# Optimization experiments

Measured on AMD Instinct MI355X. Metric: run time of the kernel, lower is better.

The kernel has to match this reference:

```python
import jax, jax.numpy as jnp
import numpy as np

B = 16384      # batch
F = 26         # onehot fields
E = 32         # embedding_dim
L = 50         # multihot bag length
V = 1000000    # num_embeddings
CT = 13        # continuous features
D0, D1, D2, D3 = 909, 512, 256, 1
LEAKY = 0.01


def _leaky(x):
    return jnp.where(x >= 0, x, LEAKY * x)


def setup_inputs() -> dict:
    key = jax.random.key(0)
    ks = jax.random.split(key, 16)
    inp = {
        "onehot_i": jax.random.randint(ks[0], (B, F), 0, V),
        "onehot_x": jax.random.uniform(ks[1], (B, F), dtype=jnp.float32),
        "multihot_i1": jax.random.randint(ks[2], (B, L), 0, V),
        "multihot_x1": jax.random.uniform(ks[3], (B, L), dtype=jnp.float32),
        "multihot_i2": jax.random.randint(ks[4], (B, L), 0, V),
        "multihot_x2": jax.random.uniform(ks[5], (B, L), dtype=jnp.float32),
        "ctns": jax.random.normal(ks[6], (B, CT), dtype=jnp.float32),
        # learned parameters
        "wide_table": jax.random.normal(ks[7], (V, 1), dtype=jnp.float32) * 0.02,
        "deep_table": jax.random.normal(ks[8], (V, E), dtype=jnp.float32) * 0.02,
        "w2": jax.random.normal(ks[9], (D1, D0), dtype=jnp.float32) * (1.0 / np.sqrt(D0)),
        "b2": jnp.zeros((D1,), dtype=jnp.float32),
        "w3": jax.random.normal(ks[10], (D2, D1), dtype=jnp.float32) * (1.0 / np.sqrt(D1)),
        "b3": jnp.zeros((D2,), dtype=jnp.float32),
        "w4": jax.random.normal(ks[11], (D3, D2), dtype=jnp.float32) * (1.0 / np.sqrt(D2)),
        "b4": jnp.zeros((D3,), dtype=jnp.float32),
    }
    return inp


def reference(onehot_i, onehot_x, multihot_i1, multihot_x1, multihot_i2,
              multihot_x2, ctns, wide_table, deep_table, w2, b2, w3, b3, w4, b4):
    # ---- wide part ----
    # Original broadcasts the [B,F,1] wide embedding against x repeated E times,
    # then sums over all columns. That equals E * sum_f(w[idx]*x).
    wide_sum = (wide_table[onehot_i, 0] * onehot_x).sum(axis=1)          # [B]
    wide_sum = wide_sum + (wide_table[multihot_i1, 0] * multihot_x1).sum(axis=1)
    wide_sum = wide_sum + (wide_table[multihot_i2, 0] * multihot_x2).sum(axis=1)
    wide_out = E * wide_sum                                              # [B]

    # ---- deep part: gather, scale by field weight, pool multihot bags ----
    d_one = (deep_table[onehot_i] * onehot_x[:, :, None]).reshape(B, F * E)   # [B, F*E]
    d_m1 = (deep_table[multihot_i1] * multihot_x1[:, :, None]).sum(axis=1)    # [B, E]
    d_m2 = (deep_table[multihot_i2] * multihot_x2[:, :, None]).sum(axis=1)    # [B, E]
    x = jnp.concatenate([d_one, d_m1, d_m2, ctns], axis=1)                    # [B, D0]

    # dropout p=0.0 (deterministic reference)
    x = _leaky(x @ w2.T + b2)
    x = _leaky(x @ w3.T + b3)
    x = (x @ w4.T + b4).squeeze(-1)                                           # [B]
    return jax.nn.sigmoid(x + wide_out)
```

## Files before the change

kernel.cpp:

```cpp
#include <hip/hip_runtime.h>
#include <hip/hip_bf16.h>
#include <math.h>

#define B_   16384
#define F_   26
#define E_   32
#define L_   50
#define CT_  13
#define D0_  909
#define D0P  928
#define D1_  512
#define D2_  256

typedef __bf16 bf16x8 __attribute__((ext_vector_type(8)));
typedef float f32x4 __attribute__((ext_vector_type(4)));

__device__ inline float bf2f(unsigned short u) {
    union { unsigned int i; float f; } v; v.i = ((unsigned int)u) << 16; return v.f;
}
__device__ inline unsigned short f2b(float f) {
    union { __hip_bfloat16 h; unsigned short u; } v;
    v.h = __float2bfloat16(f);
    return v.u;
}

__device__ inline void gld_lds16(const void* g, void* l) {
    __builtin_amdgcn_global_load_lds(
        (const __attribute__((address_space(1))) unsigned int*)g,
        (__attribute__((address_space(3))) unsigned int*)l, 16, 0, 0);
}

#define W2N (D1_ * D0P)
#define W3N (D2_ * D1_)
__global__ __launch_bounds__(256) void cvt_weights(
    const float* __restrict__ w2, const float* __restrict__ w3,
    __hip_bfloat16* __restrict__ o2, __hip_bfloat16* __restrict__ o3)
{
    int i = blockIdx.x * 256 + threadIdx.x;
    if (i < W2N) {
        int r = i / D0P, c = i - r * D0P;
        float v = (c < D0_) ? w2[r * D0_ + c] : 0.f;
        o2[i] = __float2bfloat16(v);
    } else {
        int j = i - W2N;
        if (j < W3N) o3[j] = __float2bfloat16(w3[j]);
    }
}

__global__ __launch_bounds__(256, 4) void embed_kernel(
    const int* __restrict__ oi, const float* __restrict__ ox,
    const int* __restrict__ i1, const float* __restrict__ x1,
    const int* __restrict__ i2, const float* __restrict__ x2,
    const float* __restrict__ ct, const float* __restrict__ wtab,
    const float* __restrict__ dtab,
    __hip_bfloat16* __restrict__ x0, float* __restrict__ wide)
{
    const int s    = blockIdx.x * 4 + (threadIdx.x >> 6);
    const int lane = threadIdx.x & 63;
    const int g    = lane >> 3;
    const int l    = lane & 7;
    unsigned short* xrow = (unsigned short*)(x0 + (size_t)s * D0P);
    const f32x4* dt4 = (const f32x4*)dtab;

    int koh[4]; float soh[4];
#pragma unroll
    for (int t = 0; t < 4; t++) {
        int f = g + 8 * t; bool v = (f < F_);
        koh[t] = v ? oi[s * F_ + f] : 0;
        soh[t] = v ? ox[s * F_ + f] : 0.f;
    }
    int k1[7], k2[7]; float sc1[7], sc2[7];
#pragma unroll
    for (int t = 0; t < 7; t++) {
        int j = g + 8 * t; bool v = (j < L_);
        k1[t]  = v ? i1[s * L_ + j] : 0;
        sc1[t] = v ? x1[s * L_ + j] : 0.f;
        k2[t]  = v ? i2[s * L_ + j] : 0;
        sc2[t] = v ? x2[s * L_ + j] : 0.f;
    }

    f32x4 r1[7], r2[7], roh[4];
#pragma unroll
    for (int t = 0; t < 7; t++) r1[t] = dt4[(size_t)k1[t] * 8 + l];
#pragma unroll
    for (int t = 0; t < 7; t++) r2[t] = dt4[(size_t)k2[t] * 8 + l];
#pragma unroll
    for (int t = 0; t < 4; t++) roh[t] = dt4[(size_t)koh[t] * 8 + l];

#pragma unroll
    for (int t = 0; t < 4; t++) {
        int f = g + 8 * t;
        if (f < F_) {
            ushort4 o;
            o.x = f2b(roh[t].x * soh[t]); o.y = f2b(roh[t].y * soh[t]);
            o.z = f2b(roh[t].z * soh[t]); o.w = f2b(roh[t].w * soh[t]);
            *(ushort4*)(xrow + f * E_ + l * 4) = o;
        }
    }

    f32x4 a1 = {0.f,0.f,0.f,0.f}, a2 = {0.f,0.f,0.f,0.f};
#pragma unroll
    for (int t = 0; t < 7; t++) {
        a1.x = fmaf(r1[t].x, sc1[t], a1.x); a1.y = fmaf(r1[t].y, sc1[t], a1.y);
        a1.z = fmaf(r1[t].z, sc1[t], a1.z); a1.w = fmaf(r1[t].w, sc1[t], a1.w);
        a2.x = fmaf(r2[t].x, sc2[t], a2.x); a2.y = fmaf(r2[t].y, sc2[t], a2.y);
        a2.z = fmaf(r2[t].z, sc2[t], a2.z); a2.w = fmaf(r2[t].w, sc2[t], a2.w);
    }
#pragma unroll
    for (int m = 8; m < 64; m <<= 1) {
        a1.x += __shfl_xor(a1.x, m); a1.y += __shfl_xor(a1.y, m);
        a1.z += __shfl_xor(a1.z, m); a1.w += __shfl_xor(a1.w, m);
        a2.x += __shfl_xor(a2.x, m); a2.y += __shfl_xor(a2.y, m);
        a2.z += __shfl_xor(a2.z, m); a2.w += __shfl_xor(a2.w, m);
    }
    if (g == 0) {
        ushort4 o; o.x = f2b(a1.x); o.y = f2b(a1.y); o.z = f2b(a1.z); o.w = f2b(a1.w);
        *(ushort4*)(xrow + F_ * E_ + l * 4) = o;
    }
    if (g == 1) {
        ushort4 o; o.x = f2b(a2.x); o.y = f2b(a2.y); o.z = f2b(a2.z); o.w = f2b(a2.w);
        *(ushort4*)(xrow + F_ * E_ + E_ + l * 4) = o;
    }
    if (lane < E_) {
        float v = (lane < CT_) ? ct[s * CT_ + lane] : 0.f;
        xrow[F_ * E_ + 2 * E_ + lane] = f2b(v);
    }
    float acc = 0.f;
#pragma unroll
    for (int t = lane; t < F_ + 2 * L_; t += 64) {
        int idx; float xv;
        if (t < F_)            { idx = oi[s * F_ + t];            xv = ox[s * F_ + t]; }
        else if (t < F_ + L_)  { int j = t - F_;       idx = i1[s * L_ + j]; xv = x1[s * L_ + j]; }
        else                   { int j = t - F_ - L_;  idx = i2[s * L_ + j]; xv = x2[s * L_ + j]; }
        acc += wtab[idx] * xv;
    }
    for (int o = 32; o; o >>= 1) acc += __shfl_xor(acc, o);
    if (lane == 0) wide[s] = (float)E_ * acc;
}

template<int N, int K, bool ACT>
__global__ __launch_bounds__(256) void gemm_bias(
    const __hip_bfloat16* __restrict__ A,
    const __hip_bfloat16* __restrict__ W,
    const float* __restrict__ bias,
    __hip_bfloat16* __restrict__ C, int MBLKS)
{
    __shared__ __hip_bfloat16 As[128 * 32];
    __shared__ __hip_bfloat16 Bs[128 * 32];

    const int bm   = blockIdx.x % MBLKS;
    const int bn   = blockIdx.x / MBLKS;
    const int tid  = threadIdx.x;
    const int lane = tid & 63;
    const int w    = tid >> 6;
    const int wm   = w >> 1, wn = w & 1;

    f32x4 acc[4][4] = {};

    const int srow = lane >> 2;
    const int scol = (lane & 3) * 8;
    const __hip_bfloat16* Aw0 = A + ((size_t)bm * 128 + w * 32 + srow) * K + scol;
    const __hip_bfloat16* Aw1 = Aw0 + (size_t)16 * K;
    const __hip_bfloat16* Ww0 = W + ((size_t)bn * 128 + w * 32 + srow) * K + scol;
    const __hip_bfloat16* Ww1 = Ww0 + (size_t)16 * K;
    char* AsW = (char*)As + w * 2048;
    char* BsW = (char*)Bs + w * 2048;

    const int fr = lane & 15;
    const int kg = (lane >> 4) * 8;

    for (int k0 = 0; k0 < K; k0 += 32) {
        gld_lds16(Aw0 + k0, AsW);
        gld_lds16(Aw1 + k0, AsW + 1024);
        gld_lds16(Ww0 + k0, BsW);
        gld_lds16(Ww1 + k0, BsW + 1024);
        __syncthreads();

        bf16x8 af[4], bfv[4];
#pragma unroll
        for (int i = 0; i < 4; i++)
            af[i] = *(const bf16x8*)(As + (wm * 64 + i * 16 + fr) * 32 + kg);
#pragma unroll
        for (int i = 0; i < 4; i++)
            bfv[i] = *(const bf16x8*)(Bs + (wn * 64 + i * 16 + fr) * 32 + kg);
#pragma unroll
        for (int i = 0; i < 4; i++)
#pragma unroll
            for (int j = 0; j < 4; j++)
                acc[i][j] = __builtin_amdgcn_mfma_f32_16x16x32_bf16(af[i], bfv[j], acc[i][j], 0, 0, 0);
        __syncthreads();
    }

    float bv[4];
#pragma unroll
    for (int j = 0; j < 4; j++) bv[j] = bias[bn * 128 + wn * 64 + j * 16 + fr];
    const int crow0 = bm * 128 + wm * 64 + (lane >> 4) * 4;
    const int ccol0 = bn * 128 + wn * 64 + fr;
#pragma unroll
    for (int i = 0; i < 4; i++)
#pragma unroll
        for (int j = 0; j < 4; j++)
#pragma unroll
            for (int r = 0; r < 4; r++) {
                float v = acc[i][j][r] + bv[j];
                if (ACT) v = (v >= 0.f) ? v : 0.01f * v;
                C[(size_t)(crow0 + i * 16 + r) * N + ccol0 + j * 16] = __float2bfloat16(v);
            }
}

__global__ __launch_bounds__(256) void final_kernel(
    const __hip_bfloat16* __restrict__ h2, const float* __restrict__ w4,
    const float* __restrict__ b4, const float* __restrict__ wide,
    float* __restrict__ out)
{
    const int s    = blockIdx.x * 4 + (threadIdx.x >> 6);
    const int lane = threadIdx.x & 63;
    const unsigned short* hp = (const unsigned short*)(h2 + (size_t)s * D2_);
    ushort4 hv = *(const ushort4*)(hp + lane * 4);
    float4  wv = *(const float4*)(w4 + lane * 4);
    float acc = bf2f(hv.x) * wv.x + bf2f(hv.y) * wv.y + bf2f(hv.z) * wv.z + bf2f(hv.w) * wv.w;
    for (int o = 32; o; o >>= 1) acc += __shfl_xor(acc, o);
    if (lane == 0) {
        float x = acc + b4[0] + wide[s];
        out[s] = 1.f / (1.f + expf(-x));
    }
}

extern "C" void kernel_launch(void* const* d_in, const int* in_sizes, int n_in,
                              void* d_out, int out_size, void* d_ws, size_t ws_size,
                              hipStream_t stream) {
    const int*   oi  = (const int*)  d_in[0];
    const float* ox  = (const float*)d_in[1];
    const int*   i1  = (const int*)  d_in[2];
    const float* x1  = (const float*)d_in[3];
    const int*   i2  = (const int*)  d_in[4];
    const float* x2  = (const float*)d_in[5];
    const float* ct  = (const float*)d_in[6];
    const float* wt  = (const float*)d_in[7];
    const float* dt  = (const float*)d_in[8];
    const float* w2  = (const float*)d_in[9];
    const float* b2  = (const float*)d_in[10];
    const float* w3  = (const float*)d_in[11];
    const float* b3  = (const float*)d_in[12];
    const float* w4  = (const float*)d_in[13];
    const float* b4  = (const float*)d_in[14];
    float* out = (float*)d_out;

    char* ws = (char*)d_ws;
    __hip_bfloat16* x0b = (__hip_bfloat16*)(ws);
    __hip_bfloat16* h1b = (__hip_bfloat16*)(ws + 30408704);
    __hip_bfloat16* h2b = (__hip_bfloat16*)(ws + 47185920);
    float*          wid = (float*)         (ws + 55574528);
    __hip_bfloat16* w2b = (__hip_bfloat16*)(ws + 55640064);
    __hip_bfloat16* w3b = (__hip_bfloat16*)(ws + 56590336);

    cvt_weights<<<(W2N + W3N + 255) / 256, 256, 0, stream>>>(w2, w3, w2b, w3b);
    embed_kernel<<<4096, 256, 0, stream>>>(oi, ox, i1, x1, i2, x2, ct, wt, dt, x0b, wid);
    gemm_bias<D1_, D0P, true ><<<128 * (D1_ / 128), 256, 0, stream>>>(x0b, w2b, b2, h1b, 128);
    gemm_bias<D2_, D1_, true ><<<128 * (D2_ / 128), 256, 0, stream>>>(h1b, w3b, b3, h2b, 128);
    final_kernel<<<4096, 256, 0, stream>>>(h2b, w4, b4, wid, out);
}
```

Measured before the change: 125.4 us.

## Fuse embedding gather, both MLP layers and output head into one kernel

```diff
diff --git a/kernel.cpp b/kernel.cpp
--- a/kernel.cpp
+++ b/kernel.cpp
@@ -2,22 +2,22 @@
 #include <hip/hip_bf16.h>
 #include <math.h>
 
-#define B_   16384
-#define F_   26
-#define E_   32
-#define L_   50
-#define CT_  13
-#define D0_  909
-#define D0P  928
-#define D1_  512
-#define D2_  256
+#define B_    16384
+#define F_    26
+#define E_    32
+#define L_    50
+#define CT_   13
+#define D0_   909
+#define D0P   928
+#define D1_   512
+#define D2_   256
+#define SAMP  16
+#define XPAD  936
+#define H1PAD 520
 
 typedef __bf16 bf16x8 __attribute__((ext_vector_type(8)));
 typedef float f32x4 __attribute__((ext_vector_type(4)));
 
-__device__ inline float bf2f(unsigned short u) {
-    union { unsigned int i; float f; } v; v.i = ((unsigned int)u) << 16; return v.f;
-}
 __device__ inline unsigned short f2b(float f) {
     union { __hip_bfloat16 h; unsigned short u; } v;
     v.h = __float2bfloat16(f);
@@ -30,199 +30,218 @@
         (__attribute__((address_space(3))) unsigned int*)l, 16, 0, 0);
 }
 
-#define W2N (D1_ * D0P)
-#define W3N (D2_ * D1_)
+#define W2N (29 * D1_ * 32)
+#define W3N (16 * D2_ * 32)
 __global__ __launch_bounds__(256) void cvt_weights(
     const float* __restrict__ w2, const float* __restrict__ w3,
     __hip_bfloat16* __restrict__ o2, __hip_bfloat16* __restrict__ o3)
 {
     int i = blockIdx.x * 256 + threadIdx.x;
     if (i < W2N) {
-        int r = i / D0P, c = i - r * D0P;
-        float v = (c < D0_) ? w2[r * D0_ + c] : 0.f;
+        int strip = i >> 14, rem = i & 16383;
+        int n = rem >> 5, kk = rem & 31;
+        int k = strip * 32 + kk;
+        float v = (k < D0_) ? w2[n * D0_ + k] : 0.f;
         o2[i] = __float2bfloat16(v);
     } else {
         int j = i - W2N;
-        if (j < W3N) o3[j] = __float2bfloat16(w3[j]);
-    }
-}
-
-__global__ __launch_bounds__(256, 4) void embed_kernel(
+        if (j < W3N) {
+            int strip = j >> 13, rem = j & 8191;
+            int n = rem >> 5, kk = rem & 31;
+            int k = strip * 32 + kk;
+            o3[j] = __float2bfloat16(w3[n * D1_ + k]);
+        }
+    }
+}
+
+__global__ __launch_bounds__(512, 4) void fused_kernel(
     const int* __restrict__ oi, const float* __restrict__ ox,
     const int* __restrict__ i1, const float* __restrict__ x1,
     const int* __restrict__ i2, const float* __restrict__ x2,
     const float* __restrict__ ct, const float* __restrict__ wtab,
     const float* __restrict__ dtab,
-    __hip_bfloat16* __restrict__ x0, float* __restrict__ wide)
+    const __hip_bfloat16* __restrict__ w2s, const float* __restrict__ b2,
+    const __hip_bfloat16* __restrict__ w3s, const float* __restrict__ b3,
+    const float* __restrict__ w4, const float* __restrict__ b4,
+    float* __restrict__ out)
 {
-    const int s    = blockIdx.x * 4 + (threadIdx.x >> 6);
-    const int lane = threadIdx.x & 63;
-    const int g    = lane >> 3;
-    const int l    = lane & 7;
-    unsigned short* xrow = (unsigned short*)(x0 + (size_t)s * D0P);
-    const f32x4* dt4 = (const f32x4*)dtab;
-
-    int koh[4]; float soh[4];
-#pragma unroll
-    for (int t = 0; t < 4; t++) {
-        int f = g + 8 * t; bool v = (f < F_);
-        koh[t] = v ? oi[s * F_ + f] : 0;
-        soh[t] = v ? ox[s * F_ + f] : 0.f;
-    }
-    int k1[7], k2[7]; float sc1[7], sc2[7];
-#pragma unroll
-    for (int t = 0; t < 7; t++) {
-        int j = g + 8 * t; bool v = (j < L_);
-        k1[t]  = v ? i1[s * L_ + j] : 0;
-        sc1[t] = v ? x1[s * L_ + j] : 0.f;
-        k2[t]  = v ? i2[s * L_ + j] : 0;
-        sc2[t] = v ? x2[s * L_ + j] : 0.f;
-    }
-
-    f32x4 r1[7], r2[7], roh[4];
-#pragma unroll
-    for (int t = 0; t < 7; t++) r1[t] = dt4[(size_t)k1[t] * 8 + l];
-#pragma unroll
-    for (int t = 0; t < 7; t++) r2[t] = dt4[(size_t)k2[t] * 8 + l];
-#pragma unroll
-    for (int t = 0; t < 4; t++) roh[t] = dt4[(size_t)koh[t] * 8 + l];
-
-#pragma unroll
-    for (int t = 0; t < 4; t++) {
-        int f = g + 8 * t;
-        if (f < F_) {
-            ushort4 o;
-            o.x = f2b(roh[t].x * soh[t]); o.y = f2b(roh[t].y * soh[t]);
-            o.z = f2b(roh[t].z * soh[t]); o.w = f2b(roh[t].w * soh[t]);
-            *(ushort4*)(xrow + f * E_ + l * 4) = o;
-        }
-    }
-
-    f32x4 a1 = {0.f,0.f,0.f,0.f}, a2 = {0.f,0.f,0.f,0.f};
-#pragma unroll
-    for (int t = 0; t < 7; t++) {
-        a1.x = fmaf(r1[t].x, sc1[t], a1.x); a1.y = fmaf(r1[t].y, sc1[t], a1.y);
-        a1.z = fmaf(r1[t].z, sc1[t], a1.z); a1.w = fmaf(r1[t].w, sc1[t], a1.w);
-        a2.x = fmaf(r2[t].x, sc2[t], a2.x); a2.y = fmaf(r2[t].y, sc2[t], a2.y);
-        a2.z = fmaf(r2[t].z, sc2[t], a2.z); a2.w = fmaf(r2[t].w, sc2[t], a2.w);
-    }
-#pragma unroll
-    for (int m = 8; m < 64; m <<= 1) {
-        a1.x += __shfl_xor(a1.x, m); a1.y += __shfl_xor(a1.y, m);
-        a1.z += __shfl_xor(a1.z, m); a1.w += __shfl_xor(a1.w, m);
-        a2.x += __shfl_xor(a2.x, m); a2.y += __shfl_xor(a2.y, m);
-        a2.z += __shfl_xor(a2.z, m); a2.w += __shfl_xor(a2.w, m);
-    }
-    if (g == 0) {
-        ushort4 o; o.x = f2b(a1.x); o.y = f2b(a1.y); o.z = f2b(a1.z); o.w = f2b(a1.w);
-        *(ushort4*)(xrow + F_ * E_ + l * 4) = o;
-    }
-    if (g == 1) {
-        ushort4 o; o.x = f2b(a2.x); o.y = f2b(a2.y); o.z = f2b(a2.z); o.w = f2b(a2.w);
-        *(ushort4*)(xrow + F_ * E_ + E_ + l * 4) = o;
-    }
-    if (lane < E_) {
-        float v = (lane < CT_) ? ct[s * CT_ + lane] : 0.f;
-        xrow[F_ * E_ + 2 * E_ + lane] = f2b(v);
-    }
-    float acc = 0.f;
-#pragma unroll
-    for (int t = lane; t < F_ + 2 * L_; t += 64) {
-        int idx; float xv;
-        if (t < F_)            { idx = oi[s * F_ + t];            xv = ox[s * F_ + t]; }
-        else if (t < F_ + L_)  { int j = t - F_;       idx = i1[s * L_ + j]; xv = x1[s * L_ + j]; }
-        else                   { int j = t - F_ - L_;  idx = i2[s * L_ + j]; xv = x2[s * L_ + j]; }
-        acc += wtab[idx] * xv;
-    }
-    for (int o = 32; o; o >>= 1) acc += __shfl_xor(acc, o);
-    if (lane == 0) wide[s] = (float)E_ * acc;
-}
-
-template<int N, int K, bool ACT>
-__global__ __launch_bounds__(256) void gemm_bias(
-    const __hip_bfloat16* __restrict__ A,
-    const __hip_bfloat16* __restrict__ W,
-    const float* __restrict__ bias,
-    __hip_bfloat16* __restrict__ C, int MBLKS)
-{
-    __shared__ __hip_bfloat16 As[128 * 32];
-    __shared__ __hip_bfloat16 Bs[128 * 32];
-
-    const int bm   = blockIdx.x % MBLKS;
-    const int bn   = blockIdx.x / MBLKS;
+    __shared__ __align__(16) unsigned short x0s[SAMP * XPAD];
+    __shared__ __align__(16) unsigned short wst[D1_ * 32];
+    __shared__ float parts[8][SAMP];
+    __shared__ float wides[SAMP];
+
     const int tid  = threadIdx.x;
     const int lane = tid & 63;
     const int w    = tid >> 6;
-    const int wm   = w >> 1, wn = w & 1;
-
-    f32x4 acc[4][4] = {};
-
-    const int srow = lane >> 2;
-    const int scol = (lane & 3) * 8;
-    const __hip_bfloat16* Aw0 = A + ((size_t)bm * 128 + w * 32 + srow) * K + scol;
-    const __hip_bfloat16* Aw1 = Aw0 + (size_t)16 * K;
-    const __hip_bfloat16* Ww0 = W + ((size_t)bn * 128 + w * 32 + srow) * K + scol;
-    const __hip_bfloat16* Ww1 = Ww0 + (size_t)16 * K;
-    char* AsW = (char*)As + w * 2048;
-    char* BsW = (char*)Bs + w * 2048;
+    const int sbase = blockIdx.x * SAMP;
+    const f32x4* dt4 = (const f32x4*)dtab;
+
+    {
+        const int g = lane >> 3;
+        const int l = lane & 7;
+        for (int ss = 0; ss < 2; ss++) {
+            const int m = w * 2 + ss;
+            const int s = sbase + m;
+            unsigned short* xrow = x0s + m * XPAD;
+
+            int koh[4]; float soh[4];
+#pragma unroll
+            for (int t = 0; t < 4; t++) {
+                int f = g + 8 * t; bool v = (f < F_);
+                koh[t] = v ? oi[s * F_ + f] : 0;
+                soh[t] = v ? ox[s * F_ + f] : 0.f;
+            }
+            int k1[7], k2[7]; float sc1[7], sc2[7];
+#pragma unroll
+            for (int t = 0; t < 7; t++) {
+                int j = g + 8 * t; bool v = (j < L_);
+                k1[t]  = v ? i1[s * L_ + j] : 0;
+                sc1[t] = v ? x1[s * L_ + j] : 0.f;
+                k2[t]  = v ? i2[s * L_ + j] : 0;
+                sc2[t] = v ? x2[s * L_ + j] : 0.f;
+            }
+            f32x4 r1[7], r2[7], roh[4];
+#pragma unroll
+            for (int t = 0; t < 7; t++) r1[t] = dt4[(size_t)k1[t] * 8 + l];
+#pragma unroll
+            for (int t = 0; t < 7; t++) r2[t] = dt4[(size_t)k2[t] * 8 + l];
+#pragma unroll
+            for (int t = 0; t < 4; t++) roh[t] = dt4[(size_t)koh[t] * 8 + l];
+
+#pragma unroll
+            for (int t = 0; t < 4; t++) {
+                int f = g + 8 * t;
+                if (f < F_) {
+                    ushort4 o;
+                    o.x = f2b(roh[t].x * soh[t]); o.y = f2b(roh[t].y * soh[t]);
+                    o.z = f2b(roh[t].z * soh[t]); o.w = f2b(roh[t].w * soh[t]);
+                    *(ushort4*)(xrow + f * E_ + l * 4) = o;
+                }
+            }
+            f32x4 a1 = {0.f,0.f,0.f,0.f}, a2 = {0.f,0.f,0.f,0.f};
+#pragma unroll
+            for (int t = 0; t < 7; t++) {
+                a1.x = fmaf(r1[t].x, sc1[t], a1.x); a1.y = fmaf(r1[t].y, sc1[t], a1.y);
+                a1.z = fmaf(r1[t].z, sc1[t], a1.z); a1.w = fmaf(r1[t].w, sc1[t], a1.w);
+                a2.x = fmaf(r2[t].x, sc2[t], a2.x); a2.y = fmaf(r2[t].y, sc2[t], a2.y);
+                a2.z = fmaf(r2[t].z, sc2[t], a2.z); a2.w = fmaf(r2[t].w, sc2[t], a2.w);
+            }
+#pragma unroll
+            for (int mm = 8; mm < 64; mm <<= 1) {
+                a1.x += __shfl_xor(a1.x, mm); a1.y += __shfl_xor(a1.y, mm);
+                a1.z += __shfl_xor(a1.z, mm); a1.w += __shfl_xor(a1.w, mm);
+                a2.x += __shfl_xor(a2.x, mm); a2.y += __shfl_xor(a2.y, mm);
+                a2.z += __shfl_xor(a2.z, mm); a2.w += __shfl_xor(a2.w, mm);
+            }
+            if (g == 0) {
+                ushort4 o; o.x = f2b(a1.x); o.y = f2b(a1.y); o.z = f2b(a1.z); o.w = f2b(a1.w);
+                *(ushort4*)(xrow + F_ * E_ + l * 4) = o;
+            }
+            if (g == 1) {
+                ushort4 o; o.x = f2b(a2.x); o.y = f2b(a2.y); o.z = f2b(a2.z); o.w = f2b(a2.w);
+                *(ushort4*)(xrow + F_ * E_ + E_ + l * 4) = o;
+            }
+            if (lane < 34) {
+                float v = (lane < CT_) ? ct[s * CT_ + lane] : 0.f;
+                xrow[F_ * E_ + 2 * E_ + lane] = f2b(v);
+            }
+            float acc = 0.f;
+#pragma unroll
+            for (int t = lane; t < F_ + 2 * L_; t += 64) {
+                int idx; float xv;
+                if (t < F_)            { idx = oi[s * F_ + t];           xv = ox[s * F_ + t]; }
+                else if (t < F_ + L_)  { int j = t - F_;      idx = i1[s * L_ + j]; xv = x1[s * L_ + j]; }
+                else                   { int j = t - F_ - L_; idx = i2[s * L_ + j]; xv = x2[s * L_ + j]; }
+                acc += wtab[idx] * xv;
+            }
+            for (int o = 32; o; o >>= 1) acc += __shfl_xor(acc, o);
+            if (lane == 0) wides[m] = (float)E_ * acc;
+        }
+    }
+    __syncthreads();
 
     const int fr = lane & 15;
-    const int kg = (lane >> 4) * 8;
-
-    for (int k0 = 0; k0 < K; k0 += 32) {
-        gld_lds16(Aw0 + k0, AsW);
-        gld_lds16(Aw1 + k0, AsW + 1024);
-        gld_lds16(Ww0 + k0, BsW);
-        gld_lds16(Ww1 + k0, BsW + 1024);
-        __syncthreads();
-
-        bf16x8 af[4], bfv[4];
-#pragma unroll
-        for (int i = 0; i < 4; i++)
-            af[i] = *(const bf16x8*)(As + (wm * 64 + i * 16 + fr) * 32 + kg);
-#pragma unroll
-        for (int i = 0; i < 4; i++)
-            bfv[i] = *(const bf16x8*)(Bs + (wn * 64 + i * 16 + fr) * 32 + kg);
-#pragma unroll
-        for (int i = 0; i < 4; i++)
-#pragma unroll
-            for (int j = 0; j < 4; j++)
-                acc[i][j] = __builtin_amdgcn_mfma_f32_16x16x32_bf16(af[i], bfv[j], acc[i][j], 0, 0, 0);
-        __syncthreads();
-    }
-
-    float bv[4];
-#pragma unroll
-    for (int j = 0; j < 4; j++) bv[j] = bias[bn * 128 + wn * 64 + j * 16 + fr];
-    const int crow0 = bm * 128 + wm * 64 + (lane >> 4) * 4;
-    const int ccol0 = bn * 128 + wn * 64 + fr;
-#pragma unroll
-    for (int i = 0; i < 4; i++)
-#pragma unroll
-        for (int j = 0; j < 4; j++)
+    const int kg = lane >> 4;
+    f32x4 acc1[4] = {};
+    const int nb1 = w * 64;
+    for (int ks = 0; ks < 29; ks++) {
+#pragma unroll
+        for (int r = 0; r < 4; r++)
+            gld_lds16(w2s + (size_t)ks * 16384 + w * 2048 + r * 512 + lane * 8,
+                      (char*)wst + w * 4096 + r * 1024);
+        __syncthreads();
+        bf16x8 a = *(const bf16x8*)(x0s + fr * XPAD + ks * 32 + kg * 8);
+#pragma unroll
+        for (int nj = 0; nj < 4; nj++) {
+            bf16x8 b = *(const bf16x8*)(wst + (nb1 + nj * 16 + fr) * 32 + kg * 8);
+            acc1[nj] = __builtin_amdgcn_mfma_f32_16x16x32_bf16(a, b, acc1[nj], 0, 0, 0);
+        }
+        __syncthreads();
+    }
+    {
+        const int m0 = kg * 4;
+#pragma unroll
+        for (int nj = 0; nj < 4; nj++) {
+            int n = nb1 + nj * 16 + fr;
+            float bb = b2[n];
 #pragma unroll
             for (int r = 0; r < 4; r++) {
-                float v = acc[i][j][r] + bv[j];
-                if (ACT) v = (v >= 0.f) ? v : 0.01f * v;
-                C[(size_t)(crow0 + i * 16 + r) * N + ccol0 + j * 16] = __float2bfloat16(v);
-            }
-}
-
-__global__ __launch_bounds__(256) void final_kernel(
-    const __hip_bfloat16* __restrict__ h2, const float* __restrict__ w4,
-    const float* __restrict__ b4, const float* __restrict__ wide,
-    float* __restrict__ out)
-{
-    const int s    = blockIdx.x * 4 + (threadIdx.x >> 6);
-    const int lane = threadIdx.x & 63;
-    const unsigned short* hp = (const unsigned short*)(h2 + (size_t)s * D2_);
-    ushort4 hv = *(const ushort4*)(hp + lane * 4);
-    float4  wv = *(const float4*)(w4 + lane * 4);
-    float acc = bf2f(hv.x) * wv.x + bf2f(hv.y) * wv.y + bf2f(hv.z) * wv.z + bf2f(hv.w) * wv.w;
-    for (int o = 32; o; o >>= 1) acc += __shfl_xor(acc, o);
-    if (lane == 0) {
-        float x = acc + b4[0] + wide[s];
-        out[s] = 1.f / (1.f + expf(-x));
+                float v = acc1[nj][r] + bb;
+                v = (v >= 0.f) ? v : 0.01f * v;
+                x0s[(m0 + r) * H1PAD + n] = f2b(v);
+            }
+        }
+    }
+    __syncthreads();
+
+    f32x4 acc2[2] = {};
+    const int nb2 = w * 32;
+    for (int ks = 0; ks < 16; ks++) {
+#pragma unroll
+        for (int r = 0; r < 2; r++)
+            gld_lds16(w3s + (size_t)ks * 8192 + w * 1024 + r * 512 + lane * 8,
+                      (char*)wst + w * 2048 + r * 1024);
+        __syncthreads();
+        bf16x8 a = *(const bf16x8*)(x0s + fr * H1PAD + ks * 32 + kg * 8);
+#pragma unroll
+        for (int nj = 0; nj < 2; nj++) {
+            bf16x8 b = *(const bf16x8*)(wst + (nb2 + nj * 16 + fr) * 32 + kg * 8);
+            acc2[nj] = __builtin_amdgcn_mfma_f32_16x16x32_bf16(a, b, acc2[nj], 0, 0, 0);
+        }
+        __syncthreads();
+    }
+
+    {
+        float p[4] = {0.f, 0.f, 0.f, 0.f};
+#pragma unroll
+        for (int nj = 0; nj < 2; nj++) {
+            int n = nb2 + nj * 16 + fr;
+            float bb = b3[n];
+            float wv = w4[n];
+#pragma unroll
+            for (int r = 0; r < 4; r++) {
+                float v = acc2[nj][r] + bb;
+                v = (v >= 0.f) ? v : 0.01f * v;
+                p[r] = fmaf(v, wv, p[r]);
+            }
+        }
+#pragma unroll
+        for (int mm = 1; mm < 16; mm <<= 1) {
+#pragma unroll
+            for (int r = 0; r < 4; r++) p[r] += __shfl_xor(p[r], mm);
+        }
+        if (fr == 0) {
+#pragma unroll
+            for (int r = 0; r < 4; r++) parts[w][kg * 4 + r] = p[r];
+        }
+    }
+    __syncthreads();
+    if (tid < SAMP) {
+        float x = 0.f;
+#pragma unroll
+        for (int ww = 0; ww < 8; ww++) x += parts[ww][tid];
+        x += b4[0] + wides[tid];
+        out[sbase + tid] = 1.f / (1.f + expf(-x));
     }
 }
 
@@ -247,16 +266,10 @@
     float* out = (float*)d_out;
 
     char* ws = (char*)d_ws;
-    __hip_bfloat16* x0b = (__hip_bfloat16*)(ws);
-    __hip_bfloat16* h1b = (__hip_bfloat16*)(ws + 30408704);
-    __hip_bfloat16* h2b = (__hip_bfloat16*)(ws + 47185920);
-    float*          wid = (float*)         (ws + 55574528);
-    __hip_bfloat16* w2b = (__hip_bfloat16*)(ws + 55640064);
-    __hip_bfloat16* w3b = (__hip_bfloat16*)(ws + 56590336);
-
-    cvt_weights<<<(W2N + W3N + 255) / 256, 256, 0, stream>>>(w2, w3, w2b, w3b);
-    embed_kernel<<<4096, 256, 0, stream>>>(oi, ox, i1, x1, i2, x2, ct, wt, dt, x0b, wid);
-    gemm_bias<D1_, D0P, true ><<<128 * (D1_ / 128), 256, 0, stream>>>(x0b, w2b, b2, h1b, 128);
-    gemm_bias<D2_, D1_, true ><<<128 * (D2_ / 128), 256, 0, stream>>>(h1b, w3b, b3, h2b, 128);
-    final_kernel<<<4096, 256, 0, stream>>>(h2b, w4, b4, wid, out);
-}
+    __hip_bfloat16* w2s = (__hip_bfloat16*)(ws);
+    __hip_bfloat16* w3s = (__hip_bfloat16*)(ws + 950272);
+
+    cvt_weights<<<(W2N + W3N + 255) / 256, 256, 0, stream>>>(w2, w3, w2s, w3s);
+    fused_kernel<<<B_ / SAMP, 512, 0, stream>>>(oi, ox, i1, x1, i2, x2, ct, wt, dt,
+                                                w2s, b2, w3s, b3, w4, b4, out);
+}
```

New measurement: 132.6 us. 5.7% more time.
